# Performance work log

Measured on AMD Instinct MI355X. Metric: run time of the kernel, lower is better.

The kernel has to match this reference:

```python
import jax, jax.numpy as jnp
import numpy as np

N = 20000   # nodes
E = 640000  # edges
F = 128     # input feature dim
H1 = 64     # hidden1
H2 = 32     # hidden2 (forced by Bilinear(32,32,1))
R = 65      # num_relations / num classes
B = 4096    # query pairs


def rgcn_conv(x, src, dst, etype, W, Wroot, b):
    """PyG RGCNConv with aggr='mean': out_i = sum_r mean_{j in N_r(i)} x_j @ W_r + x_i @ Wroot + b."""
    n, f = x.shape
    seg = dst * R + etype                      # combined (node, relation) segment id
    msgs = x[src]                              # [E, f] gather
    agg = jax.ops.segment_sum(msgs, seg, num_segments=n * R).reshape(n, R, f)
    cnt = jax.ops.segment_sum(jnp.ones((msgs.shape[0],), x.dtype), seg, num_segments=n * R).reshape(n, R, 1)
    mean = agg / jnp.maximum(cnt, 1.0)         # mean per relation, zero where no edges
    out = jnp.einsum('nrf,rfo->no', mean, W) + x @ Wroot + b
    return out


def bilinear(h, c, w, b):
    # torch.nn.Bilinear(32,32,1): w [1,32,32], b [1]
    return jnp.einsum('nh,hk,nk->n', h, w[0], c)[:, None] + b


def setup_inputs():
    key = jax.random.key(0)
    ks = jax.random.split(key, 20)
    inp = {}
    inp['x_o'] = jax.random.normal(ks[0], (N, F), jnp.float32)
    inp['x_a'] = jax.random.normal(ks[1], (N, F), jnp.float32)
    inp['edge_index'] = jax.random.randint(ks[2], (2, E), 0, N, dtype=jnp.int32)
    inp['e_type'] = jax.random.randint(ks[3], (E,), 0, R, dtype=jnp.int32)
    inp['e_type1'] = jax.random.randint(ks[4], (E,), 0, R, dtype=jnp.int32)
    inp['idx'] = jax.random.randint(ks[5], (2, B), 0, N, dtype=jnp.int32)
    # RGCN layer 1
    s1 = 1.0 / np.sqrt(F)
    inp['W1'] = jax.random.normal(ks[6], (R, F, H1), jnp.float32) * s1
    inp['root1'] = jax.random.normal(ks[7], (F, H1), jnp.float32) * s1
    inp['b1'] = jnp.zeros((H1,), jnp.float32)
    # RGCN layer 2
    s2 = 1.0 / np.sqrt(H1)
    inp['W2'] = jax.random.normal(ks[8], (R, H1, H2), jnp.float32) * s2
    inp['root2'] = jax.random.normal(ks[9], (H1, H2), jnp.float32) * s2
    inp['b2'] = jnp.zeros((H2,), jnp.float32)
    # attention mix, discriminator, classifier
    inp['attt'] = jnp.array([0.5, 0.5], jnp.float32)
    inp['disc_w'] = jax.random.normal(ks[10], (1, H2, H2), jnp.float32) * (1.0 / np.sqrt(H2))
    inp['disc_b'] = jnp.zeros((1,), jnp.float32)
    cin = 2 * (H1 + H2)
    inp['cls_w'] = jax.random.normal(ks[11], (cin, R), jnp.float32) * (1.0 / np.sqrt(cin))
    inp['cls_b'] = jnp.zeros((R,), jnp.float32)
    return inp


def reference(x_o, x_a, edge_index, e_type, e_type1, idx,
              W1, root1, b1, W2, root2, b2, attt, disc_w, disc_b, cls_w, cls_b):
    src, dst = edge_index[0], edge_index[1]
    # three encoder passes (dropout is identity at eval)
    x1_o = jax.nn.relu(rgcn_conv(x_o, src, dst, e_type, W1, root1, b1))
    x2_o = rgcn_conv(x1_o, src, dst, e_type, W2, root2, b2)

    x1_a = jax.nn.relu(rgcn_conv(x_a, src, dst, e_type, W1, root1, b1))
    x2_o_a = rgcn_conv(x1_a, src, dst, e_type, W2, root2, b2)

    x1_aa = jax.nn.relu(rgcn_conv(x_o, src, dst, e_type1, W1, root1, b1))
    x2_o_a_a = rgcn_conv(x1_aa, src, dst, e_type1, W2, root2, b2)

    # readout + sigmoid, expanded summary vector
    h_os = jax.nn.sigmoid(jnp.mean(x2_o, axis=0))        # [H2]
    c_x = jnp.broadcast_to(h_os, x2_o.shape)             # [N, H2]
    ret_os = jnp.concatenate([bilinear(x2_o, c_x, disc_w, disc_b),
                              bilinear(x2_o_a, c_x, disc_w, disc_b)], axis=1)
    ret_os_a = jnp.concatenate([bilinear(x2_o, c_x, disc_w, disc_b),
                                bilinear(x2_o_a_a, c_x, disc_w, disc_b)], axis=1)

    final = jnp.concatenate([attt[0] * x1_o, attt[1] * x2_o], axis=1)  # [N, H1+H2]
    entity1 = final[idx[0]]
    entity2 = final[idx[1]]
    concat = jnp.concatenate([entity1, entity2], axis=1)  # [B, 2*(H1+H2)]
    log = concat @ cls_w + cls_b                           # [B, 65]
    return (log, ret_os, ret_os_a, x2_o)
```

## Files before the change

kernel.cpp:

```cpp
#include <hip/hip_runtime.h>

#define NN 20000
#define NE 640000
#define FF 128
#define H1 64
#define H2 32
#define RR 65
#define BQ 4096
#define NDPAD 20480

#define SM_HIST_A 0
#define SM_START_A 128
#define SM_CUR_A 256
#define SM_HIST_B 384
#define SM_START_B 512
#define SM_CUR_B 640
#define SM_HACC 768
#define SM_V 832

#define CPB1 32
#define CPB2 32

typedef __attribute__((ext_vector_type(8))) short bhalf8;
typedef __attribute__((ext_vector_type(4))) float f32x4;
// ... 1 lines not shown

__device__ __forceinline__ unsigned short f2bf(float f) {
  unsigned int u = __float_as_uint(f);
  unsigned int r = (u + 0x7fffu + ((u >> 16) & 1u)) >> 16;
  return (unsigned short)r;
}
__device__ __forceinline__ float bf2f(unsigned short u) {
  return __uint_as_float((unsigned)u << 16);
}
__device__ __forceinline__ void atomPK(unsigned short* p, unsigned v) {
  asm volatile("global_atomic_pk_add_bf16 %0, %1, off"
               :: "v"((unsigned long long)p), "v"(v) : "memory");
}

__global__ __launch_bounds__(256) void k_hist(
    const int* __restrict__ ei, const int* __restrict__ etA, const int* __restrict__ etB,
    int* __restrict__ sm, int* __restrict__ cntD) {
  __shared__ int lh[2 * RR];
  int tid = threadIdx.x;
  for (int i = tid; i < 2 * RR; i += blockDim.x) lh[i] = 0;
  __syncthreads();
  int e = blockIdx.x * blockDim.x + tid;
  if (e < NE) {
    int dst = ei[NE + e];
    atomicAdd(&cntD[dst], 1);
    atomicAdd(&lh[etA[e]], 1);
    atomicAdd(&lh[RR + etB[e]], 1);
  }
  __syncthreads();
  for (int i = tid; i < 2 * RR; i += blockDim.x) {
    int c = lh[i];
    if (c) atomicAdd(&sm[(i < RR) ? (SM_HIST_A + i) : (SM_HIST_B + (i - RR))], c);
  }
}

__global__ __launch_bounds__(128) void k_prefix(int* __restrict__ sm) {
  int w = threadIdx.x >> 6;
  if ((threadIdx.x & 63) == 0 && w < 2) {
    int hb = w ? SM_HIST_B : SM_HIST_A;
    int sb = w ? SM_START_B : SM_START_A;
    int cb = w ? SM_CUR_B : SM_CUR_A;
    int h[RR];
#pragma unroll
    for (int r = 0; r < RR; ++r) h[r] = sm[hb + r];
    int s = 0;
#pragma unroll
    for (int r = 0; r < RR; ++r) { sm[sb + r] = s; sm[cb + r] = s; s += h[r]; }
  }
}

__global__ __launch_bounds__(256) void k_prefixD(
    const int* __restrict__ cntD, int* __restrict__ startD,
    int* __restrict__ curA, int* __restrict__ curB) {
  __shared__ int psum[256];
  __shared__ int pbase[257];
  int t = threadIdx.x;
  int c0 = t * 80;
  int c1 = (c0 + 80 < NN) ? (c0 + 80) : NN;
  int s = 0;
  for (int i = c0; i < c1; ++i) s += cntD[i];
  psum[t] = s;
  __syncthreads();
  if (t == 0) {
    int a = 0;
    for (int i = 0; i < 256; ++i) { pbase[i] = a; a += psum[i]; }
    pbase[256] = a;
  }
  __syncthreads();
  int run = pbase[t];
  for (int i = c0; i < c1; ++i) {
    startD[i] = run; curA[i] = run; curB[i] = run;
    run += cntD[i];
  }
  if (t == 255) startD[NN] = pbase[256];
}

__global__ __launch_bounds__(256) void k_scatter(
    const int* __restrict__ etA, const int* __restrict__ etB,
    int* __restrict__ sm, int* __restrict__ ordA, int* __restrict__ ordB) {
  __shared__ int lhA[RR], lbA[RR], lhB[RR], lbB[RR];
  int tid = threadIdx.x;
  for (int i = tid; i < RR; i += blockDim.x) { lhA[i] = 0; lhB[i] = 0; }
  __syncthreads();
  int e = blockIdx.x * blockDim.x + tid;
  int ta = 0, tb = 0, ra = 0, rb = 0;
  bool valid = (e < NE);
  if (valid) {
    ta = etA[e]; tb = etB[e];
    ra = atomicAdd(&lhA[ta], 1);
    rb = atomicAdd(&lhB[tb], 1);
  }
  __syncthreads();
  for (int i = tid; i < RR; i += blockDim.x) {
    if (lhA[i]) lbA[i] = atomicAdd(&sm[SM_CUR_A + i], lhA[i]);
    if (lhB[i]) lbB[i] = atomicAdd(&sm[SM_CUR_B + i], lhB[i]);
  }
  __syncthreads();
  if (valid) { ordA[lbA[ta] + ra] = e; ordB[lbB[tb] + rb] = e; }
}

__global__ __launch_bounds__(256) void k_emeta(
    const int* __restrict__ ei, const int* __restrict__ ordA, const int* __restrict__ ordB,
    const int* __restrict__ etA, const int* __restrict__ etB,
    int2* __restrict__ sdA, int2* __restrict__ sdB) {
  int p = blockIdx.x * blockDim.x + threadIdx.x;
  if (p >= NE) return;
  {
    int e = ordA[p];
    sdA[p] = make_int2(ei[e] | (etA[e] << 20), ei[NE + e]);
  }
  {
    int e = ordB[p];
    sdB[p] = make_int2(ei[e] | (etB[e] << 20), ei[NE + e]);
  }
}

__global__ __launch_bounds__(256) void k_scatterD(
    const int2* __restrict__ sdA, const int2* __restrict__ sdB,
    int* __restrict__ curA, int* __restrict__ curB,
    int* __restrict__ posA, int* __restrict__ posB) {
  int p = blockIdx.x * blockDim.x + threadIdx.x;
  if (p >= NE) return;
  posA[atomicAdd(&curA[sdA[p].y], 1)] = p;
  posB[atomicAdd(&curB[sdB[p].y], 1)] = p;
}

__global__ __launch_bounds__(256) void k_invD(
    const int* __restrict__ startD, const int* __restrict__ pos,
    const int2* __restrict__ sd, float* __restrict__ iv) {
  int lane = threadIdx.x & 63;
  int d = (blockIdx.x * blockDim.x + threadIdx.x) >> 6;
  if (d >= NN) return;
  int e0 = startD[d], e1 = startD[d + 1];
  int len = e1 - e0;
  for (int c0 = 0; c0 < len; c0 += 64) {
    int myj = c0 + lane;
    int myp = 0, myrel = -1;
    if (myj < len) { myp = pos[e0 + myj]; myrel = ((unsigned)sd[myp].x) >> 20; }
    int cnt = 0;
    for (int c1 = 0; c1 < len; c1 += 64) {
      int oj = c1 + lane;
      int orel = (oj < len) ? (int)(((unsigned)sd[pos[e0 + oj]].x) >> 20) : -2;
      int kmax = (len - c1 < 64) ? (len - c1) : 64;
      for (int k = 0; k < kmax; ++k)
        cnt += (__shfl(orel, k) == myrel);
    }
    if (myj < len) iv[myp] = 1.0f / (float)cnt;
  }
}

__global__ __launch_bounds__(256) void k_cvt2(const float4* __restrict__ inA,
                                              const float4* __restrict__ inB,
                                              uint4* __restrict__ outA,
                                              uint4* __restrict__ outB, int n8) {
  int i = blockIdx.x * blockDim.x + threadIdx.x;
  if (i >= 2 * n8) return;
  const float4* in = (i < n8) ? inA : inB;
  uint4* out = (i < n8) ? outA : outB;
  int j = (i < n8) ? i : i - n8;
  float4 a = in[2 * j], b = in[2 * j + 1];
  uint4 o;
  o.x = (unsigned)f2bf(a.x) | ((unsigned)f2bf(a.y) << 16);
  o.y = (unsigned)f2bf(a.z) | ((unsigned)f2bf(a.w) << 16);
  o.z = (unsigned)f2bf(b.x) | ((unsigned)f2bf(b.y) << 16);
  o.w = (unsigned)f2bf(b.z) | ((unsigned)f2bf(b.w) << 16);
  out[j] = o;
}

__global__ __launch_bounds__(256) void k_relu16(uint4* __restrict__ a, int n4) {
  int i = blockIdx.x * blockDim.x + threadIdx.x;
// ... 53 lines not shown
#pragma unroll
  for (int j = 0; j < FF / 4; ++j) {
    float vo[4], va[4];
    *(float4*)vo = xo4[j];
    *(float4*)va = xa4[j];
#pragma unroll
    for (int t = 0; t < 4; ++t) {
      float wv = rt[(4 * j + t) * H1 + lane];
      so = fmaf(vo[t], wv, so);
      sa = fmaf(va[t], wv, sa);
    }
  }
  yo[(size_t)n * H1 + lane] = f2bf(so);
  yaa[(size_t)n * H1 + lane] = f2bf(so);
  ya[(size_t)n * H1 + lane] = f2bf(sa);
}

#define LM(G, SD, IV)                                       \
  {                                                         \
    const int base_ = s0 + ((G) << 4);                      \
    const int lim_ = cnt - ((G) << 4);                      \
    const int off_ = base_ + ((col < lim_) ? col : 0);      \
    SD = sdp[off_];                                         \
    IV = (col < lim_) ? invp[off_] : 0.f;                   \
  }

#define MFMA_BODY1(A0, A1, A2, A3)                                  \
  f32x4 c0 = {0.f,0.f,0.f,0.f}, c1 = c0, c2 = c0, c3 = c0;          \
  c0 = MFMA16(A0, wb[0], c0);  c1 = MFMA16(A0, wb[1], c1);          \
  c2 = MFMA16(A0, wb[2], c2);  c3 = MFMA16(A0, wb[3], c3);          \
  c0 = MFMA16(A1, wb[4], c0);  c1 = MFMA16(A1, wb[5], c1);          \
  c2 = MFMA16(A1, wb[6], c2);  c3 = MFMA16(A1, wb[7], c3);          \
  c0 = MFMA16(A2, wb[8], c0);  c1 = MFMA16(A2, wb[9], c1);          \
  c2 = MFMA16(A2, wb[10], c2); c3 = MFMA16(A2, wb[11], c3);         \
  c0 = MFMA16(A3, wb[12], c0); c1 = MFMA16(A3, wb[13], c1);         \
  c2 = MFMA16(A3, wb[14], c2); c3 = MFMA16(A3, wb[15], c3);

template <int NIN>
__global__ __launch_bounds__(256, 2) void k_edge1m(
    const int2* __restrict__ sdp, const float* __restrict__ invp,
    const int* __restrict__ sm, int startOff, int histOff,
    const unsigned short* __restrict__ Wf,
    const unsigned short* __restrict__ x16A, const unsigned short* __restrict__ x16B,
    unsigned short* __restrict__ yA, unsigned short* __restrict__ yB) {
  const int r = blockIdx.x / CPB1;
  const int lane = threadIdx.x & 63;
  bhalf8 wb[16];
  {
    const bhalf8* wf = (const bhalf8*)Wf + ((size_t)r * 16) * 64 + lane;
#pragma unroll
    for (int s = 0; s < 16; ++s) wb[s] = wf[(size_t)s * 64];
  }
  const int wvid = (blockIdx.x - r * CPB1) * 4 + (threadIdx.x >> 6);
  const int stride = CPB1 * 4;
  const int s0 = sm[startOff + r];
  const int cnt = sm[histOff + r];
  const int ngroups = (cnt + 15) >> 4;
  if (wvid >= ngroups) return;
  const int cg = lane >> 4;
  const int col = lane & 15;
  const int row0 = cg << 2;

  int2 sdC; float ivC;
  LM(wvid, sdC, ivC);
  for (int G = wvid; G < ngroups; G += stride) {
    int2 sdN = sdC; float ivN = ivC;
    if (G + stride < ngroups) LM(G + stride, sdN, ivN);
    const int src = sdC.x & 0xFFFFF;
    const int dstv = sdC.y;
    const int d0 = __shfl(dstv, row0),     d1 = __shfl(dstv, row0 + 1),
              d2 = __shfl(dstv, row0 + 2), d3 = __shfl(dstv, row0 + 3);
    const float i0 = __shfl(ivC, row0),     i1 = __shfl(ivC, row0 + 1),
                i2 = __shfl(ivC, row0 + 2), i3 = __shfl(ivC, row0 + 3);
#define SCAT1(Y, CCN, NOFF)                                                     \
    {                                                                           \
      float v0 = (CCN)[0] * i0, v1 = (CCN)[1] * i1,                             \
            v2 = (CCN)[2] * i2, v3 = (CCN)[3] * i3;                             \
      float p0 = __shfl_xor(v0, 1), p1 = __shfl_xor(v1, 1),                     \
            p2 = __shfl_xor(v2, 1), p3 = __shfl_xor(v3, 1);                     \
      if (!(lane & 1)) {                                                        \
        atomPK(Y + (size_t)d0 * H1 + (NOFF) + col, (unsigned)f2bf(v0) | ((unsigned)f2bf(p0) << 16)); \
        atomPK(Y + (size_t)d1 * H1 + (NOFF) + col, (unsigned)f2bf(v1) | ((unsigned)f2bf(p1) << 16)); \
        atomPK(Y + (size_t)d2 * H1 + (NOFF) + col, (unsigned)f2bf(v2) | ((unsigned)f2bf(p2) << 16)); \
        atomPK(Y + (size_t)d3 * H1 + (NOFF) + col, (unsigned)f2bf(v3) | ((unsigned)f2bf(p3) << 16)); \
      }                                                                         \
    }
    {
      const bhalf8* xr = (const bhalf8*)x16A + ((size_t)src << 4);
      bhalf8 a0 = xr[cg], a1 = xr[4 + cg], a2 = xr[8 + cg], a3 = xr[12 + cg];
      MFMA_BODY1(a0, a1, a2, a3)
      SCAT1(yA, c0, 0); SCAT1(yA, c1, 16); SCAT1(yA, c2, 32); SCAT1(yA, c3, 48);
    }
    if constexpr (NIN == 2) {
      const bhalf8* xr = (const bhalf8*)x16B + ((size_t)src << 4);
      bhalf8 a0 = xr[cg], a1 = xr[4 + cg], a2 = xr[8 + cg], a3 = xr[12 + cg];
      MFMA_BODY1(a0, a1, a2, a3)
      SCAT1(yB, c0, 0); SCAT1(yB, c1, 16); SCAT1(yB, c2, 32); SCAT1(yB, c3, 48);
    }
#undef SCAT1
    sdC = sdN; ivC = ivN;
  }
}

template <int NIN>
__global__ __launch_bounds__(256, 2) void k_edge1s(
    const int2* __restrict__ sdp, const float* __restrict__ invp,
    const int* __restrict__ sm, int startOff, int histOff,
    const unsigned short* __restrict__ Wf,
    const unsigned short* __restrict__ x16A, const unsigned short* __restrict__ x16B,
    unsigned short* __restrict__ tA, unsigned short* __restrict__ tB) {
  const int r = blockIdx.x / CPB1;
  const int lane = threadIdx.x & 63;
  bhalf8 wb[16];
  {
    const bhalf8* wf = (const bhalf8*)Wf + ((size_t)r * 16) * 64 + lane;
#pragma unroll
    for (int s = 0; s < 16; ++s) wb[s] = wf[(size_t)s * 64];
  }
  const int wvid = (blockIdx.x - r * CPB1) * 4 + (threadIdx.x >> 6);
  const int stride = CPB1 * 4;
  const int s0 = sm[startOff + r];
  const int cnt = sm[histOff + r];
  const int ngroups = (cnt + 15) >> 4;
  if (wvid >= ngroups) return;
  const int cg = lane >> 4;
  const int col = lane & 15;
  const int row0 = cg << 2;

  int2 sdC; float ivC;
  LM(wvid, sdC, ivC);
  for (int G = wvid; G < ngroups; G += stride) {
    int2 sdN = sdC; float ivN = ivC;
    if (G + stride < ngroups) LM(G + stride, sdN, ivN);
    const int src = sdC.x & 0xFFFFF;
    const int base = s0 + (G << 4);
    const int lim = cnt - (G << 4);
    const float i0 = __shfl(ivC, row0),     i1 = __shfl(ivC, row0 + 1),
                i2 = __shfl(ivC, row0 + 2), i3 = __shfl(ivC, row0 + 3);
#define STOR1(T, CCN, NOFF)                                                     \
    {                                                                           \
      float v0 = (CCN)[0] * i0, v1 = (CCN)[1] * i1,                             \
            v2 = (CCN)[2] * i2, v3 = (CCN)[3] * i3;                             \
      float p0 = __shfl_xor(v0, 1), p1 = __shfl_xor(v1, 1),                     \
            p2 = __shfl_xor(v2, 1), p3 = __shfl_xor(v3, 1);                     \
      if (!(lane & 1)) {                                                        \
        if (row0 + 0 < lim) *(unsigned*)(T + (size_t)(base + row0 + 0) * H1 + (NOFF) + col) = (unsigned)f2bf(v0) | ((unsigned)f2bf(p0) << 16); \
        if (row0 + 1 < lim) *(unsigned*)(T + (size_t)(base + row0 + 1) * H1 + (NOFF) + col) = (unsigned)f2bf(v1) | ((unsigned)f2bf(p1) << 16); \
        if (row0 + 2 < lim) *(unsigned*)(T + (size_t)(base + row0 + 2) * H1 + (NOFF) + col) = (unsigned)f2bf(v2) | ((unsigned)f2bf(p2) << 16); \
        if (row0 + 3 < lim) *(unsigned*)(T + (size_t)(base + row0 + 3) * H1 + (NOFF) + col) = (unsigned)f2bf(v3) | ((unsigned)f2bf(p3) << 16); \
      }                                                                         \
    }
    {
      const bhalf8* xr = (const bhalf8*)x16A + ((size_t)src << 4);
      bhalf8 a0 = xr[cg], a1 = xr[4 + cg], a2 = xr[8 + cg], a3 = xr[12 + cg];
      MFMA_BODY1(a0, a1, a2, a3)
      STOR1(tA, c0, 0); STOR1(tA, c1, 16); STOR1(tA, c2, 32); STOR1(tA, c3, 48);
    }
    if constexpr (NIN == 2) {
      const bhalf8* xr = (const bhalf8*)x16B + ((size_t)src << 4);
      bhalf8 a0 = xr[cg], a1 = xr[4 + cg], a2 = xr[8 + cg], a3 = xr[12 + cg];
      MFMA_BODY1(a0, a1, a2, a3)
      STOR1(tB, c0, 0); STOR1(tB, c1, 16); STOR1(tB, c2, 32); STOR1(tB, c3, 48);
    }
#undef STOR1
    sdC = sdN; ivC = ivN;
  }
}

template <int NT>
__global__ __launch_bounds__(256) void k_reduce1(
    const int* __restrict__ startD, const int* __restrict__ pos,
    const unsigned short* __restrict__ t0, const unsigned short* __restrict__ t1,
    const unsigned short* __restrict__ r0, const unsigned short* __restrict__ r1,
    unsigned short* __restrict__ y0, unsigned short* __restrict__ y1) {
  int lane = threadIdx.x & 63;
  int d = (blockIdx.x * blockDim.x + threadIdx.x) >> 6;
  if (d >= NN) return;
  int e0 = startD[d], e1 = startD[d + 1];
  float a0 = 0.f, a1 = 0.f;
  int j = e0;
  for (; j + 4 <= e1; j += 4) {
    int p0 = pos[j], p1 = pos[j + 1], p2 = pos[j + 2], p3 = pos[j + 3];
    a0 += bf2f(t0[(size_t)p0 * H1 + lane]) + bf2f(t0[(size_t)p1 * H1 + lane])
        + bf2f(t0[(size_t)p2 * H1 + lane]) + bf2f(t0[(size_t)p3 * H1 + lane]);
    if constexpr (NT == 2)
      a1 += bf2f(t1[(size_t)p0 * H1 + lane]) + bf2f(t1[(size_t)p1 * H1 + lane])
          + bf2f(t1[(size_t)p2 * H1 + lane]) + bf2f(t1[(size_t)p3 * H1 + lane]);
  }
  for (; j < e1; ++j) {
    int p = pos[j];
    a0 += bf2f(t0[(size_t)p * H1 + lane]);
    if constexpr (NT == 2) a1 += bf2f(t1[(size_t)p * H1 + lane]);
  }
  size_t o = (size_t)d * H1 + lane;
  y0[o] = f2bf(fmaxf(bf2f(r0[o]) + a0, 0.f));
  if constexpr (NT == 2) y1[o] = f2bf(fmaxf(bf2f(r1[o]) + a1, 0.f));
}

__global__ __launch_bounds__(256) void k_root2x3(
    const unsigned short* __restrict__ x1o, const unsigned short* __restrict__ x1a,
    const unsigned short* __restrict__ x1aa,
    const float* __restrict__ rt, const float* __restrict__ b,
    unsigned short* __restrict__ y0, unsigned short* __restrict__ y1,
    unsigned short* __restrict__ y2) {
  int i = blockIdx.x * blockDim.x + threadIdx.x;
  if (i >= NN * H2) return;
  int o = i & (H2 - 1);
  int n = i >> 5;
  const uint2* p0 = (const uint2*)(x1o + (size_t)n * H1);
  const uint2* p1 = (const uint2*)(x1a + (size_t)n * H1);
  const uint2* p2 = (const uint2*)(x1aa + (size_t)n * H1);
  float s0 = b[o], s1 = s0, s2 = s0;
#pragma unroll
  for (int j = 0; j < 16; ++j) {
    uint2 u0 = p0[j], u1 = p1[j], u2 = p2[j];
#pragma unroll
    for (int t = 0; t < 4; ++t) {
      unsigned w0 = (t < 2) ? u0.x : u0.y;
      unsigned w1 = (t < 2) ? u1.x : u1.y;
      unsigned w2 = (t < 2) ? u2.x : u2.y;
      int sh = (t & 1) * 16;
      float wv = rt[(4 * j + t) * H2 + o];
      s0 = fmaf(bf2f((unsigned short)(w0 >> sh)), wv, s0);
      s1 = fmaf(bf2f((unsigned short)(w1 >> sh)), wv, s1);
      s2 = fmaf(bf2f((unsigned short)(w2 >> sh)), wv, s2);
    }
  }
  y0[i] = f2bf(s0); y1[i] = f2bf(s1); y2[i] = f2bf(s2);
}

template <int NIN>
__global__ __launch_bounds__(256, 2) void k_edge2m(
    const int2* __restrict__ sdp, const float* __restrict__ invp,
    const int* __restrict__ sm, int startOff, int histOff,
    const unsigned short* __restrict__ Wf,
    const unsigned short* __restrict__ x16A, const unsigned short* __restrict__ x16B,
    unsigned short* __restrict__ yA, unsigned short* __restrict__ yB) {
  const int r = blockIdx.x / CPB2;
  const int lane = threadIdx.x & 63;
  bhalf8 wb[4];
  {
    const bhalf8* wf = (const bhalf8*)Wf + ((size_t)r * 4) * 64 + lane;
#pragma unroll
    for (int s = 0; s < 4; ++s) wb[s] = wf[(size_t)s * 64];
  }
  const int wvid = (blockIdx.x - r * CPB2) * 4 + (threadIdx.x >> 6);
  const int stride = CPB2 * 4;
  const int s0 = sm[startOff + r];
  const int cnt = sm[histOff + r];
  const int ngroups = (cnt + 15) >> 4;
  if (wvid >= ngroups) return;
  const int cg = lane >> 4;
  const int col = lane & 15;
  const int row0 = cg << 2;

  int2 sdC; float ivC;
  LM(wvid, sdC, ivC);
  for (int G = wvid; G < ngroups; G += stride) {
    int2 sdN = sdC; float ivN = ivC;
    if (G + stride < ngroups) LM(G + stride, sdN, ivN);
    const int src = sdC.x & 0xFFFFF;
    const int dstv = sdC.y;
    const int d0 = __shfl(dstv, row0),     d1 = __shfl(dstv, row0 + 1),
              d2 = __shfl(dstv, row0 + 2), d3 = __shfl(dstv, row0 + 3);
    const float i0 = __shfl(ivC, row0),     i1 = __shfl(ivC, row0 + 1),
                i2 = __shfl(ivC, row0 + 2), i3 = __shfl(ivC, row0 + 3);
#define SCAT2(Y, CCN, NOFF)                                                     \
    {                                                                           \
      float v0 = (CCN)[0] * i0, v1 = (CCN)[1] * i1,                             \
            v2 = (CCN)[2] * i2, v3 = (CCN)[3] * i3;                             \
      float p0 = __shfl_xor(v0, 1), p1 = __shfl_xor(v1, 1),                     \
            p2 = __shfl_xor(v2, 1), p3 = __shfl_xor(v3, 1);                     \
      if (!(lane & 1)) {                                                        \
        atomPK(Y + (size_t)d0 * H2 + (NOFF) + col, (unsigned)f2bf(v0) | ((unsigned)f2bf(p0) << 16)); \
        atomPK(Y + (size_t)d1 * H2 + (NOFF) + col, (unsigned)f2bf(v1) | ((unsigned)f2bf(p1) << 16)); \
        atomPK(Y + (size_t)d2 * H2 + (NOFF) + col, (unsigned)f2bf(v2) | ((unsigned)f2bf(p2) << 16)); \
        atomPK(Y + (size_t)d3 * H2 + (NOFF) + col, (unsigned)f2bf(v3) | ((unsigned)f2bf(p3) << 16)); \
      }                                                                         \
    }
    {
      const bhalf8* xr = (const bhalf8*)x16A + ((size_t)src << 3);
      bhalf8 a0 = xr[cg], a1 = xr[4 + cg];
      f32x4 c0 = {0.f,0.f,0.f,0.f}, c1 = c0;
      c0 = MFMA16(a0, wb[0], c0); c1 = MFMA16(a0, wb[1], c1);
      c0 = MFMA16(a1, wb[2], c0); c1 = MFMA16(a1, wb[3], c1);
      SCAT2(yA, c0, 0); SCAT2(yA, c1, 16);
    }
    if constexpr (NIN == 2) {
      const bhalf8* xr = (const bhalf8*)x16B + ((size_t)src << 3);
      bhalf8 a0 = xr[cg], a1 = xr[4 + cg];
      f32x4 c0 = {0.f,0.f,0.f,0.f}, c1 = c0;
      c0 = MFMA16(a0, wb[0], c0); c1 = MFMA16(a0, wb[1], c1);
      c0 = MFMA16(a1, wb[2], c0); c1 = MFMA16(a1, wb[3], c1);
      SCAT2(yB, c0, 0); SCAT2(yB, c1, 16);
    }
#undef SCAT2
    sdC = sdN; ivC = ivN;
  }
}

template <int NIN>
__global__ __launch_bounds__(256, 2) void k_edge2s(
    const int2* __restrict__ sdp, const float* __restrict__ invp,
    const int* __restrict__ sm, int startOff, int histOff,
    const unsigned short* __restrict__ Wf,
    const unsigned short* __restrict__ x16A, const unsigned short* __restrict__ x16B,
    unsigned short* __restrict__ tA, unsigned short* __restrict__ tB) {
  const int r = blockIdx.x / CPB2;
  const int lane = threadIdx.x & 63;
  bhalf8 wb[4];
  {
    const bhalf8* wf = (const bhalf8*)Wf + ((size_t)r * 4) * 64 + lane;
#pragma unroll
    for (int s = 0; s < 4; ++s) wb[s] = wf[(size_t)s * 64];
  }
  const int wvid = (blockIdx.x - r * CPB2) * 4 + (threadIdx.x >> 6);
  const int stride = CPB2 * 4;
  const int s0 = sm[startOff + r];
  const int cnt = sm[histOff + r];
  const int ngroups = (cnt + 15) >> 4;
  if (wvid >= ngroups) return;
  const int cg = lane >> 4;
  const int col = lane & 15;
  const int row0 = cg << 2;

  int2 sdC; float ivC;
  LM(wvid, sdC, ivC);
  for (int G = wvid; G < ngroups; G += stride) {
    int2 sdN = sdC; float ivN = ivC;
    if (G + stride < ngroups) LM(G + stride, sdN, ivN);
    const int src = sdC.x & 0xFFFFF;
    const int base = s0 + (G << 4);
    const int lim = cnt - (G << 4);
    const float i0 = __shfl(ivC, row0),     i1 = __shfl(ivC, row0 + 1),
                i2 = __shfl(ivC, row0 + 2), i3 = __shfl(ivC, row0 + 3);
#define STOR2(T, CCN, NOFF)                                                     \
    {                                                                           \
      float v0 = (CCN)[0] * i0, v1 = (CCN)[1] * i1,                             \
            v2 = (CCN)[2] * i2, v3 = (CCN)[3] * i3;                             \
      float p0 = __shfl_xor(v0, 1), p1 = __shfl_xor(v1, 1),                     \
            p2 = __shfl_xor(v2, 1), p3 = __shfl_xor(v3, 1);                     \
      if (!(lane & 1)) {                                                        \
        if (row0 + 0 < lim) *(unsigned*)(T + (size_t)(base + row0 + 0) * H2 + (NOFF) + col) = (unsigned)f2bf(v0) | ((unsigned)f2bf(p0) << 16); \
        if (row0 + 1 < lim) *(unsigned*)(T + (size_t)(base + row0 + 1) * H2 + (NOFF) + col) = (unsigned)f2bf(v1) | ((unsigned)f2bf(p1) << 16); \
        if (row0 + 2 < lim) *(unsigned*)(T + (size_t)(base + row0 + 2) * H2 + (NOFF) + col) = (unsigned)f2bf(v2) | ((unsigned)f2bf(p2) << 16); \
        if (row0 + 3 < lim) *(unsigned*)(T + (size_t)(base + row0 + 3) * H2 + (NOFF) + col) = (unsigned)f2bf(v3) | ((unsigned)f2bf(p3) << 16); \
      }                                                                         \
    }
    {
      const bhalf8* xr = (const bhalf8*)x16A + ((size_t)src << 3);
      bhalf8 a0 = xr[cg], a1 = xr[4 + cg];
      f32x4 c0 = {0.f,0.f,0.f,0.f}, c1 = c0;
      c0 = MFMA16(a0, wb[0], c0); c1 = MFMA16(a0, wb[1], c1);
      c0 = MFMA16(a1, wb[2], c0); c1 = MFMA16(a1, wb[3], c1);
      STOR2(tA, c0, 0); STOR2(tA, c1, 16);
    }
    if constexpr (NIN == 2) {
      const bhalf8* xr = (const bhalf8*)x16B + ((size_t)src << 3);
      bhalf8 a0 = xr[cg], a1 = xr[4 + cg];
      f32x4 c0 = {0.f,0.f,0.f,0.f}, c1 = c0;
      c0 = MFMA16(a0, wb[0], c0); c1 = MFMA16(a0, wb[1], c1);
      c0 = MFMA16(a1, wb[2], c0); c1 = MFMA16(a1, wb[3], c1);
      STOR2(tB, c0, 0); STOR2(tB, c1, 16);
    }
#undef STOR2
    sdC = sdN; ivC = ivN;
  }
}

template <int NT>
__global__ __launch_bounds__(256) void k_reduce2(
    const int* __restrict__ startD, const int* __restrict__ pos,
    const unsigned short* __restrict__ t0, const unsigned short* __restrict__ t1,
    const unsigned short* __restrict__ r0, const unsigned short* __restrict__ r1,
    unsigned short* __restrict__ y0, unsigned short* __restrict__ y1,
    float* __restrict__ f32out) {
  int gt = blockIdx.x * blockDim.x + threadIdx.x;
  int d = gt >> 5;
  int colc = gt & 31;
  if (d >= NN) return;
  int e0 = startD[d], e1 = startD[d + 1];
  float a0 = 0.f, a1 = 0.f;
  int j = e0;
  for (; j + 4 <= e1; j += 4) {
    int p0 = pos[j], p1 = pos[j + 1], p2 = pos[j + 2], p3 = pos[j + 3];
    a0 += bf2f(t0[(size_t)p0 * H2 + colc]) + bf2f(t0[(size_t)p1 * H2 + colc])
        + bf2f(t0[(size_t)p2 * H2 + colc]) + bf2f(t0[(size_t)p3 * H2 + colc]);
    if constexpr (NT == 2)
      a1 += bf2f(t1[(size_t)p0 * H2 + colc]) + bf2f(t1[(size_t)p1 * H2 + colc])
          + bf2f(t1[(size_t)p2 * H2 + colc]) + bf2f(t1[(size_t)p3 * H2 + colc]);
  }
  for (; j < e1; ++j) {
    int p = pos[j];
    a0 += bf2f(t0[(size_t)p * H2 + colc]);
    if constexpr (NT == 2) a1 += bf2f(t1[(size_t)p * H2 + colc]);
  }
  size_t o = (size_t)d * H2 + colc;
  float v0 = bf2f(r0[o]) + a0;
  y0[o] = f2bf(v0);
  if (f32out) f32out[o] = v0;
  if constexpr (NT == 2) y1[o] = f2bf(bf2f(r1[o]) + a1);
}

__global__ __launch_bounds__(256) void k_fin(const uint4* __restrict__ xb,
                                             float4* __restrict__ out, int n8) {
  int i = blockIdx.x * blockDim.x + threadIdx.x;
  if (i >= n8) return;
  uint4 u = xb[i];
  float4 a, b;
  a.x = bf2f((unsigned short)u.x); a.y = bf2f((unsigned short)(u.x >> 16));
  a.z = bf2f((unsigned short)u.y); a.w = bf2f((unsigned short)(u.y >> 16));
  b.x = bf2f((unsigned short)u.z); b.y = bf2f((unsigned short)(u.z >> 16));
  b.z = bf2f((unsigned short)u.w); b.w = bf2f((unsigned short)(u.w >> 16));
  out[2 * i] = a; out[2 * i + 1] = b;
}

__global__ __launch_bounds__(256) void k_colsum(const float* __restrict__ x2o,
                                                float* __restrict__ hacc) {
// ... 104 lines not shown
                              hipStream_t stream) {
  const float* x_o  = (const float*)d_in[0];
  const float* x_a  = (const float*)d_in[1];
  const int*   ei   = (const int*)d_in[2];
  const int*   etA  = (const int*)d_in[3];
  const int*   etB  = (const int*)d_in[4];
  const int*   idx  = (const int*)d_in[5];
  const float* W1   = (const float*)d_in[6];
  const float* rt1  = (const float*)d_in[7];
  const float* b1   = (const float*)d_in[8];
  const float* W2   = (const float*)d_in[9];
  const float* rt2  = (const float*)d_in[10];
  const float* b2   = (const float*)d_in[11];
  const float* attt = (const float*)d_in[12];
  const float* dw   = (const float*)d_in[13];
  const float* db   = (const float*)d_in[14];
  const float* cw   = (const float*)d_in[15];
  const float* cb   = (const float*)d_in[16];

  int* wsI    = (int*)d_ws;
  int* sm     = wsI;
  int* cntD   = sm + 1024;
  int* startD = cntD + NDPAD;
  int* curA   = startD + NDPAD;
  int* curB   = curA + NDPAD;
  int* ordA   = curB + NDPAD;
  int* ordB   = ordA + NE;
  int* posA   = ordB + NE;
  int* posB   = posA + NE;
  int2*  sdA  = (int2*)(posB + NE);
  int2*  sdB  = sdA + NE;
  float* ivA  = (float*)(sdB + NE);
  float* ivB  = ivA + NE;
  unsigned short* x1o16   = (unsigned short*)(ivB + NE);
  unsigned short* x1a16   = x1o16 + (size_t)NN * H1;
  unsigned short* x1aa16  = x1a16 + (size_t)NN * H1;
  unsigned short* x2ob    = x1aa16 + (size_t)NN * H1;
  unsigned short* x2oab   = x2ob + (size_t)NN * H2;
  unsigned short* x2oaab  = x2oab + (size_t)NN * H2;
  unsigned short* xo16    = x2oaab + (size_t)NN * H2;
  unsigned short* xa16    = xo16 + (size_t)NN * FF;
  unsigned short* W1f     = xa16 + (size_t)NN * FF;
  unsigned short* W2f     = W1f + (size_t)RR * 16 * 64 * 8;
  unsigned short* rootO16 = W2f + (size_t)RR * 4 * 64 * 8;
  unsigned short* rootA16 = rootO16 + (size_t)NN * H1;
  unsigned short* r2o16   = rootA16 + (size_t)NN * H1;
  unsigned short* r2a16   = r2o16 + (size_t)NN * H2;
  unsigned short* r2aa16  = r2a16 + (size_t)NN * H2;
  unsigned short* t0      = r2aa16 + (size_t)NN * H2;
  unsigned short* t1      = t0 + (size_t)NE * H1;
  unsigned short* tc1     = t0 + (size_t)NE * H2;

  const size_t ofsT = (size_t)((char*)t0 - (char*)d_ws);
  const size_t needFull = ofsT + (size_t)2 * NE * H1 * 2 + 256;
  const size_t needMid  = ofsT + (size_t)2 * NE * H2 * 2 + 256;
  const bool fullT = ws_size >= needFull;
  const bool midT  = fullT || ws_size >= needMid;

  float* smF  = (float*)sm;
  float* hacc = smF + SM_HACC;
  float* vbuf = smF + SM_V;

  float* outF   = (float*)d_out;
  float* o_log  = outF;
  float* o_ros  = outF + (size_t)BQ * RR;
  float* o_rosa = o_ros + (size_t)NN * 2;
  float* o_x2o  = o_rosa + (size_t)NN * 2;

  hipMemsetAsync(wsI, 0, (1024 + NDPAD) * sizeof(int), stream);

  k_cvt2<<<(2 * NN * FF / 8 + 255) / 256, 256, 0, stream>>>(
      (const float4*)x_o, (const float4*)x_a, (uint4*)xo16, (uint4*)xa16, NN * FF / 8);
  k_wprep1<<<RR, 256, 0, stream>>>(W1, W1f);
  k_wprep2<<<RR, 256, 0, stream>>>(W2, W2f);

  k_hist<<<(NE + 255) / 256, 256, 0, stream>>>(ei, etA, etB, sm, cntD);
  k_prefix<<<1, 128, 0, stream>>>(sm);
  k_prefixD<<<1, 256, 0, stream>>>(cntD, startD, curA, curB);
  k_scatter<<<(NE + 255) / 256, 256, 0, stream>>>(etA, etB, sm, ordA, ordB);
  k_emeta<<<(NE + 255) / 256, 256, 0, stream>>>(ei, ordA, ordB, etA, etB, sdA, sdB);
  k_scatterD<<<(NE + 255) / 256, 256, 0, stream>>>(sdA, sdB, curA, curB, posA, posB);
  k_invD<<<(NN * 64 + 255) / 256, 256, 0, stream>>>(startD, posA, sdA, ivA);
  k_invD<<<(NN * 64 + 255) / 256, 256, 0, stream>>>(startD, posB, sdB, ivB);

  if (fullT) {
    k_root1<<<(NN * H1) / 256, 256, 0, stream>>>(x_o, x_a, rt1, b1,
                                                 rootO16, rootO16, rootA16);
    k_edge1s<2><<<RR * CPB1, 256, 0, stream>>>(sdA, ivA, sm, SM_START_A, SM_HIST_A,
                                               W1f, xo16, xa16, t0, t1);
    k_reduce1<2><<<(NN * 64) / 256, 256, 0, stream>>>(startD, posA, t0, t1,
                                                      rootO16, rootA16, x1o16, x1a16);
    k_edge1s<1><<<RR * CPB1, 256, 0, stream>>>(sdB, ivB, sm, SM_START_B, SM_HIST_B,
                                               W1f, xo16, nullptr, t0, nullptr);
    k_reduce1<1><<<(NN * 64) / 256, 256, 0, stream>>>(startD, posB, t0, nullptr,
                                                      rootO16, nullptr, x1aa16, nullptr);
  } else {
    k_root1<<<(NN * H1) / 256, 256, 0, stream>>>(x_o, x_a, rt1, b1,
                                                 x1o16, x1aa16, x1a16);
    k_edge1m<2><<<RR * CPB1, 256, 0, stream>>>(sdA, ivA, sm, SM_START_A, SM_HIST_A,
                                               W1f, xo16, xa16, x1o16, x1a16);
    k_edge1m<1><<<RR * CPB1, 256, 0, stream>>>(sdB, ivB, sm, SM_START_B, SM_HIST_B,
                                               W1f, xo16, nullptr, x1aa16, nullptr);
    k_relu16<<<(3 * NN * H1 / 8 + 255) / 256, 256, 0, stream>>>((uint4*)x1o16,
                                                                3 * NN * H1 / 8);
  }

  if (midT) {
    k_root2x3<<<(NN * H2 + 255) / 256, 256, 0, stream>>>(x1o16, x1a16, x1aa16, rt2, b2,
                                                         r2o16, r2a16, r2aa16);
    k_edge2s<2><<<RR * CPB2, 256, 0, stream>>>(sdA, ivA, sm, SM_START_A, SM_HIST_A,
                                               W2f, x1o16, x1a16, t0, tc1);
    k_reduce2<2><<<(NN * 32) / 256, 256, 0, stream>>>(startD, posA, t0, tc1,
                                                      r2o16, r2a16, x2ob, x2oab, o_x2o);
    k_edge2s<1><<<RR * CPB2, 256, 0, stream>>>(sdB, ivB, sm, SM_START_B, SM_HIST_B,
                                               W2f, x1aa16, nullptr, t0, nullptr);
    k_reduce2<1><<<(NN * 32) / 256, 256, 0, stream>>>(startD, posB, t0, nullptr,
                                                      r2aa16, nullptr, x2oaab, nullptr,
                                                      nullptr);
  } else {
    k_root2x3<<<(NN * H2 + 255) / 256, 256, 0, stream>>>(x1o16, x1a16, x1aa16, rt2, b2,
                                                         x2ob, x2oab, x2oaab);
    k_edge2m<2><<<RR * CPB2, 256, 0, stream>>>(sdA, ivA, sm, SM_START_A, SM_HIST_A,
                                               W2f, x1o16, x1a16, x2ob, x2oab);
    k_edge2m<1><<<RR * CPB2, 256, 0, stream>>>(sdB, ivB, sm, SM_START_B, SM_HIST_B,
                                               W2f, x1aa16, nullptr, x2oaab, nullptr);
    k_fin<<<(NN * H2 / 8 + 255) / 256, 256, 0, stream>>>((const uint4*)x2ob,
                                                         (float4*)o_x2o, NN * H2 / 8);
  }

  k_colsum<<<128, 256, 0, stream>>>(o_x2o, hacc);
  k_disc<<<1, 64, 0, stream>>>(hacc, dw, vbuf);
  k_ret<<<(NN + 255) / 256, 256, 0, stream>>>(x2ob, x2oab, x2oaab, vbuf, db, o_ros, o_rosa);
  k_cls<<<BQ, 128, 0, stream>>>(idx, x1o16, o_x2o, attt, cw, cb, o_log);
}
```

Measured before the change: 828.1 us.

## Fuse edge preprocessing into one scatter with shared destination-slot index

Replaces the scatter, edge-metadata, destination-scatter and two inverse-count kernels with a single fused scatter. That scatter assigns each edge one destination-sorted slot q and packs src and dst into 15 bits each. Edge kernels write messages directly to slot q, so the reduce kernels read contiguous rows instead of chasing a pos indirection. A combined relation array lets one pass compute the inverse counts for both edge-type sets. This removes several launches and indirect loads, in exchange for scattered stores in the edge kernels and a 15-bit packing limit on node ids.

```diff
diff --git a/kernel.cpp b/kernel.cpp
--- a/kernel.cpp
+++ b/kernel.cpp
@@ -47,8 +47,7 @@
   __syncthreads();
   int e = blockIdx.x * blockDim.x + tid;
   if (e < NE) {
-    int dst = ei[NE + e];
-    atomicAdd(&cntD[dst], 1);
+    atomicAdd(&cntD[ei[NE + e]], 1);
     atomicAdd(&lh[etA[e]], 1);
     atomicAdd(&lh[RR + etB[e]], 1);
   }
@@ -75,8 +74,7 @@
 }
 
 __global__ __launch_bounds__(256) void k_prefixD(
-    const int* __restrict__ cntD, int* __restrict__ startD,
-    int* __restrict__ curA, int* __restrict__ curB) {
+    const int* __restrict__ cntD, int* __restrict__ startD, int* __restrict__ cur) {
   __shared__ int psum[256];
   __shared__ int pbase[257];
   int t = threadIdx.x;
@@ -94,15 +92,17 @@
   __syncthreads();
   int run = pbase[t];
   for (int i = c0; i < c1; ++i) {
-    startD[i] = run; curA[i] = run; curB[i] = run;
+    startD[i] = run; cur[i] = run;
     run += cntD[i];
   }
   if (t == 255) startD[NN] = pbase[256];
 }
 
-__global__ __launch_bounds__(256) void k_scatter(
-    const int* __restrict__ etA, const int* __restrict__ etB,
-    int* __restrict__ sm, int* __restrict__ ordA, int* __restrict__ ordB) {
+__global__ __launch_bounds__(256) void k_scatterF(
+    const int* __restrict__ ei, const int* __restrict__ etA, const int* __restrict__ etB,
+    int* __restrict__ sm, int* __restrict__ cur,
+    int2* __restrict__ sdA, int2* __restrict__ sdB,
+    unsigned short* __restrict__ relQ) {
   __shared__ int lhA[RR], lbA[RR], lhB[RR], lbB[RR];
   int tid = threadIdx.x;
   for (int i = tid; i < RR; i += blockDim.x) { lhA[i] = 0; lhB[i] = 0; }
@@ -121,38 +121,19 @@
     if (lhB[i]) lbB[i] = atomicAdd(&sm[SM_CUR_B + i], lhB[i]);
   }
   __syncthreads();
-  if (valid) { ordA[lbA[ta] + ra] = e; ordB[lbB[tb] + rb] = e; }
-}
-
-__global__ __launch_bounds__(256) void k_emeta(
-    const int* __restrict__ ei, const int* __restrict__ ordA, const int* __restrict__ ordB,
-    const int* __restrict__ etA, const int* __restrict__ etB,
-    int2* __restrict__ sdA, int2* __restrict__ sdB) {
-  int p = blockIdx.x * blockDim.x + threadIdx.x;
-  if (p >= NE) return;
-  {
-    int e = ordA[p];
-    sdA[p] = make_int2(ei[e] | (etA[e] << 20), ei[NE + e]);
-  }
-  {
-    int e = ordB[p];
-    sdB[p] = make_int2(ei[e] | (etB[e] << 20), ei[NE + e]);
-  }
-}
-
-__global__ __launch_bounds__(256) void k_scatterD(
-    const int2* __restrict__ sdA, const int2* __restrict__ sdB,
-    int* __restrict__ curA, int* __restrict__ curB,
-    int* __restrict__ posA, int* __restrict__ posB) {
-  int p = blockIdx.x * blockDim.x + threadIdx.x;
-  if (p >= NE) return;
-  posA[atomicAdd(&curA[sdA[p].y], 1)] = p;
-  posB[atomicAdd(&curB[sdB[p].y], 1)] = p;
-}
-
-__global__ __launch_bounds__(256) void k_invD(
-    const int* __restrict__ startD, const int* __restrict__ pos,
-    const int2* __restrict__ sd, float* __restrict__ iv) {
+  if (valid) {
+    int src = ei[e], dst = ei[NE + e];
+    int q = atomicAdd(&cur[dst], 1);
+    int packed = src | (dst << 15);
+    sdA[lbA[ta] + ra] = make_int2(packed, q);
+    sdB[lbB[tb] + rb] = make_int2(packed, q);
+    relQ[q] = (unsigned short)(ta | (tb << 8));
+  }
+}
+
+__global__ __launch_bounds__(256) void k_invD2(
+    const int* __restrict__ startD, const unsigned short* __restrict__ relQ,
+    float* __restrict__ ivqA, float* __restrict__ ivqB) {
   int lane = threadIdx.x & 63;
   int d = (blockIdx.x * blockDim.x + threadIdx.x) >> 6;
   if (d >= NN) return;
@@ -160,17 +141,23 @@
   int len = e1 - e0;
   for (int c0 = 0; c0 < len; c0 += 64) {
     int myj = c0 + lane;
-    int myp = 0, myrel = -1;
-    if (myj < len) { myp = pos[e0 + myj]; myrel = ((unsigned)sd[myp].x) >> 20; }
-    int cnt = 0;
+    int mr = (myj < len) ? (int)relQ[e0 + myj] : 0;
+    int mA = mr & 0xFF, mB = mr >> 8;
+    int cA = 0, cB = 0;
     for (int c1 = 0; c1 < len; c1 += 64) {
       int oj = c1 + lane;
-      int orel = (oj < len) ? (int)(((unsigned)sd[pos[e0 + oj]].x) >> 20) : -2;
+      int orr = (oj < len) ? (int)relQ[e0 + oj] : 0;
       int kmax = (len - c1 < 64) ? (len - c1) : 64;
-      for (int k = 0; k < kmax; ++k)
-        cnt += (__shfl(orel, k) == myrel);
-    }
-    if (myj < len) iv[myp] = 1.0f / (float)cnt;
+      for (int k = 0; k < kmax; ++k) {
+        int o = __shfl(orr, k);
+        cA += ((o & 0xFF) == mA);
+        cB += ((o >> 8) == mB);
+      }
+    }
+    if (myj < len) {
+      ivqA[e0 + myj] = 1.0f / (float)cA;
+      ivqB[e0 + myj] = 1.0f / (float)cB;
+    }
   }
 }
 
@@ -270,7 +257,7 @@
     const int lim_ = cnt - ((G) << 4);                      \
     const int off_ = base_ + ((col < lim_) ? col : 0);      \
     SD = sdp[off_];                                         \
-    IV = (col < lim_) ? invp[off_] : 0.f;                   \
+    IV = (col < lim_) ? ivq[SD.y] : 0.f;                    \
   }
 
 #define MFMA_BODY1(A0, A1, A2, A3)                                  \
@@ -286,7 +273,7 @@
 
 template <int NIN>
 __global__ __launch_bounds__(256, 2) void k_edge1m(
-    const int2* __restrict__ sdp, const float* __restrict__ invp,
+    const int2* __restrict__ sdp, const float* __restrict__ ivq,
     const int* __restrict__ sm, int startOff, int histOff,
     const unsigned short* __restrict__ Wf,
     const unsigned short* __restrict__ x16A, const unsigned short* __restrict__ x16B,
@@ -314,8 +301,8 @@
   for (int G = wvid; G < ngroups; G += stride) {
     int2 sdN = sdC; float ivN = ivC;
     if (G + stride < ngroups) LM(G + stride, sdN, ivN);
-    const int src = sdC.x & 0xFFFFF;
-    const int dstv = sdC.y;
+    const int src = sdC.x & 0x7FFF;
+    const int dstv = (sdC.x >> 15) & 0x7FFF;
     const int d0 = __shfl(dstv, row0),     d1 = __shfl(dstv, row0 + 1),
               d2 = __shfl(dstv, row0 + 2), d3 = __shfl(dstv, row0 + 3);
     const float i0 = __shfl(ivC, row0),     i1 = __shfl(ivC, row0 + 1),
@@ -352,7 +339,7 @@
 
 template <int NIN>
 __global__ __launch_bounds__(256, 2) void k_edge1s(
-    const int2* __restrict__ sdp, const float* __restrict__ invp,
+    const int2* __restrict__ sdp, const float* __restrict__ ivq,
     const int* __restrict__ sm, int startOff, int histOff,
     const unsigned short* __restrict__ Wf,
     const unsigned short* __restrict__ x16A, const unsigned short* __restrict__ x16B,
@@ -380,9 +367,11 @@
   for (int G = wvid; G < ngroups; G += stride) {
     int2 sdN = sdC; float ivN = ivC;
     if (G + stride < ngroups) LM(G + stride, sdN, ivN);
-    const int src = sdC.x & 0xFFFFF;
-    const int base = s0 + (G << 4);
+    const int src = sdC.x & 0x7FFF;
+    const int qv = sdC.y;
     const int lim = cnt - (G << 4);
+    const int q0 = __shfl(qv, row0),     q1 = __shfl(qv, row0 + 1),
+              q2 = __shfl(qv, row0 + 2), q3 = __shfl(qv, row0 + 3);
     const float i0 = __shfl(ivC, row0),     i1 = __shfl(ivC, row0 + 1),
                 i2 = __shfl(ivC, row0 + 2), i3 = __shfl(ivC, row0 + 3);
 #define STOR1(T, CCN, NOFF)                                                     \
@@ -392,10 +381,10 @@
       float p0 = __shfl_xor(v0, 1), p1 = __shfl_xor(v1, 1),                     \
             p2 = __shfl_xor(v2, 1), p3 = __shfl_xor(v3, 1);                     \
       if (!(lane & 1)) {                                                        \
-        if (row0 + 0 < lim) *(unsigned*)(T + (size_t)(base + row0 + 0) * H1 + (NOFF) + col) = (unsigned)f2bf(v0) | ((unsigned)f2bf(p0) << 16); \
-        if (row0 + 1 < lim) *(unsigned*)(T + (size_t)(base + row0 + 1) * H1 + (NOFF) + col) = (unsigned)f2bf(v1) | ((unsigned)f2bf(p1) << 16); \
-        if (row0 + 2 < lim) *(unsigned*)(T + (size_t)(base + row0 + 2) * H1 + (NOFF) + col) = (unsigned)f2bf(v2) | ((unsigned)f2bf(p2) << 16); \
-        if (row0 + 3 < lim) *(unsigned*)(T + (size_t)(base + row0 + 3) * H1 + (NOFF) + col) = (unsigned)f2bf(v3) | ((unsigned)f2bf(p3) << 16); \
+        if (row0 + 0 < lim) *(unsigned*)(T + (size_t)q0 * H1 + (NOFF) + col) = (unsigned)f2bf(v0) | ((unsigned)f2bf(p0) << 16); \
+        if (row0 + 1 < lim) *(unsigned*)(T + (size_t)q1 * H1 + (NOFF) + col) = (unsigned)f2bf(v1) | ((unsigned)f2bf(p1) << 16); \
+        if (row0 + 2 < lim) *(unsigned*)(T + (size_t)q2 * H1 + (NOFF) + col) = (unsigned)f2bf(v2) | ((unsigned)f2bf(p2) << 16); \
+        if (row0 + 3 < lim) *(unsigned*)(T + (size_t)q3 * H1 + (NOFF) + col) = (unsigned)f2bf(v3) | ((unsigned)f2bf(p3) << 16); \
       }                                                                         \
     }
     {
@@ -417,7 +406,7 @@
 
 template <int NT>
 __global__ __launch_bounds__(256) void k_reduce1(
-    const int* __restrict__ startD, const int* __restrict__ pos,
+    const int* __restrict__ startD,
     const unsigned short* __restrict__ t0, const unsigned short* __restrict__ t1,
     const unsigned short* __restrict__ r0, const unsigned short* __restrict__ r1,
     unsigned short* __restrict__ y0, unsigned short* __restrict__ y1) {
@@ -426,19 +415,9 @@
   if (d >= NN) return;
   int e0 = startD[d], e1 = startD[d + 1];
   float a0 = 0.f, a1 = 0.f;
-  int j = e0;
-  for (; j + 4 <= e1; j += 4) {
-    int p0 = pos[j], p1 = pos[j + 1], p2 = pos[j + 2], p3 = pos[j + 3];
-    a0 += bf2f(t0[(size_t)p0 * H1 + lane]) + bf2f(t0[(size_t)p1 * H1 + lane])
-        + bf2f(t0[(size_t)p2 * H1 + lane]) + bf2f(t0[(size_t)p3 * H1 + lane]);
-    if constexpr (NT == 2)
-      a1 += bf2f(t1[(size_t)p0 * H1 + lane]) + bf2f(t1[(size_t)p1 * H1 + lane])
-          + bf2f(t1[(size_t)p2 * H1 + lane]) + bf2f(t1[(size_t)p3 * H1 + lane]);
-  }
-  for (; j < e1; ++j) {
-    int p = pos[j];
-    a0 += bf2f(t0[(size_t)p * H1 + lane]);
-    if constexpr (NT == 2) a1 += bf2f(t1[(size_t)p * H1 + lane]);
+  for (int j = e0; j < e1; ++j) {
+    a0 += bf2f(t0[(size_t)j * H1 + lane]);
+    if constexpr (NT == 2) a1 += bf2f(t1[(size_t)j * H1 + lane]);
   }
   size_t o = (size_t)d * H1 + lane;
   y0[o] = f2bf(fmaxf(bf2f(r0[o]) + a0, 0.f));
@@ -479,7 +458,7 @@
 
 template <int NIN>
 __global__ __launch_bounds__(256, 2) void k_edge2m(
-    const int2* __restrict__ sdp, const float* __restrict__ invp,
+    const int2* __restrict__ sdp, const float* __restrict__ ivq,
     const int* __restrict__ sm, int startOff, int histOff,
     const unsigned short* __restrict__ Wf,
     const unsigned short* __restrict__ x16A, const unsigned short* __restrict__ x16B,
@@ -507,8 +486,8 @@
   for (int G = wvid; G < ngroups; G += stride) {
     int2 sdN = sdC; float ivN = ivC;
     if (G + stride < ngroups) LM(G + stride, sdN, ivN);
-    const int src = sdC.x & 0xFFFFF;
-    const int dstv = sdC.y;
+    const int src = sdC.x & 0x7FFF;
+    const int dstv = (sdC.x >> 15) & 0x7FFF;
     const int d0 = __shfl(dstv, row0),     d1 = __shfl(dstv, row0 + 1),
               d2 = __shfl(dstv, row0 + 2), d3 = __shfl(dstv, row0 + 3);
     const float i0 = __shfl(ivC, row0),     i1 = __shfl(ivC, row0 + 1),
@@ -549,7 +528,7 @@
 
 template <int NIN>
 __global__ __launch_bounds__(256, 2) void k_edge2s(
-    const int2* __restrict__ sdp, const float* __restrict__ invp,
+    const int2* __restrict__ sdp, const float* __restrict__ ivq,
     const int* __restrict__ sm, int startOff, int histOff,
     const unsigned short* __restrict__ Wf,
     const unsigned short* __restrict__ x16A, const unsigned short* __restrict__ x16B,
@@ -577,9 +556,11 @@
   for (int G = wvid; G < ngroups; G += stride) {
     int2 sdN = sdC; float ivN = ivC;
     if (G + stride < ngroups) LM(G + stride, sdN, ivN);
-    const int src = sdC.x & 0xFFFFF;
-    const int base = s0 + (G << 4);
+    const int src = sdC.x & 0x7FFF;
+    const int qv = sdC.y;
     const int lim = cnt - (G << 4);
+    const int q0 = __shfl(qv, row0),     q1 = __shfl(qv, row0 + 1),
+              q2 = __shfl(qv, row0 + 2), q3 = __shfl(qv, row0 + 3);
     const float i0 = __shfl(ivC, row0),     i1 = __shfl(ivC, row0 + 1),
                 i2 = __shfl(ivC, row0 + 2), i3 = __shfl(ivC, row0 + 3);
 #define STOR2(T, CCN, NOFF)                                                     \
@@ -589,10 +570,10 @@
       float p0 = __shfl_xor(v0, 1), p1 = __shfl_xor(v1, 1),                     \
             p2 = __shfl_xor(v2, 1), p3 = __shfl_xor(v3, 1);                     \
       if (!(lane & 1)) {                                                        \
-        if (row0 + 0 < lim) *(unsigned*)(T + (size_t)(base + row0 + 0) * H2 + (NOFF) + col) = (unsigned)f2bf(v0) | ((unsigned)f2bf(p0) << 16); \
-        if (row0 + 1 < lim) *(unsigned*)(T + (size_t)(base + row0 + 1) * H2 + (NOFF) + col) = (unsigned)f2bf(v1) | ((unsigned)f2bf(p1) << 16); \
-        if (row0 + 2 < lim) *(unsigned*)(T + (size_t)(base + row0 + 2) * H2 + (NOFF) + col) = (unsigned)f2bf(v2) | ((unsigned)f2bf(p2) << 16); \
-        if (row0 + 3 < lim) *(unsigned*)(T + (size_t)(base + row0 + 3) * H2 + (NOFF) + col) = (unsigned)f2bf(v3) | ((unsigned)f2bf(p3) << 16); \
+        if (row0 + 0 < lim) *(unsigned*)(T + (size_t)q0 * H2 + (NOFF) + col) = (unsigned)f2bf(v0) | ((unsigned)f2bf(p0) << 16); \
+        if (row0 + 1 < lim) *(unsigned*)(T + (size_t)q1 * H2 + (NOFF) + col) = (unsigned)f2bf(v1) | ((unsigned)f2bf(p1) << 16); \
+        if (row0 + 2 < lim) *(unsigned*)(T + (size_t)q2 * H2 + (NOFF) + col) = (unsigned)f2bf(v2) | ((unsigned)f2bf(p2) << 16); \
+        if (row0 + 3 < lim) *(unsigned*)(T + (size_t)q3 * H2 + (NOFF) + col) = (unsigned)f2bf(v3) | ((unsigned)f2bf(p3) << 16); \
       }                                                                         \
     }
     {
@@ -618,7 +599,7 @@
 
 template <int NT>
 __global__ __launch_bounds__(256) void k_reduce2(
-    const int* __restrict__ startD, const int* __restrict__ pos,
+    const int* __restrict__ startD,
     const unsigned short* __restrict__ t0, const unsigned short* __restrict__ t1,
     const unsigned short* __restrict__ r0, const unsigned short* __restrict__ r1,
     unsigned short* __restrict__ y0, unsigned short* __restrict__ y1,
@@ -629,19 +610,9 @@
   if (d >= NN) return;
   int e0 = startD[d], e1 = startD[d + 1];
   float a0 = 0.f, a1 = 0.f;
-  int j = e0;
-  for (; j + 4 <= e1; j += 4) {
-    int p0 = pos[j], p1 = pos[j + 1], p2 = pos[j + 2], p3 = pos[j + 3];
-    a0 += bf2f(t0[(size_t)p0 * H2 + colc]) + bf2f(t0[(size_t)p1 * H2 + colc])
-        + bf2f(t0[(size_t)p2 * H2 + colc]) + bf2f(t0[(size_t)p3 * H2 + colc]);
-    if constexpr (NT == 2)
-      a1 += bf2f(t1[(size_t)p0 * H2 + colc]) + bf2f(t1[(size_t)p1 * H2 + colc])
-          + bf2f(t1[(size_t)p2 * H2 + colc]) + bf2f(t1[(size_t)p3 * H2 + colc]);
-  }
-  for (; j < e1; ++j) {
-    int p = pos[j];
-    a0 += bf2f(t0[(size_t)p * H2 + colc]);
-    if constexpr (NT == 2) a1 += bf2f(t1[(size_t)p * H2 + colc]);
+  for (int j = e0; j < e1; ++j) {
+    a0 += bf2f(t0[(size_t)j * H2 + colc]);
+    if constexpr (NT == 2) a1 += bf2f(t1[(size_t)j * H2 + colc]);
   }
   size_t o = (size_t)d * H2 + colc;
   float v0 = bf2f(r0[o]) + a0;
@@ -792,17 +763,13 @@
   int* sm     = wsI;
   int* cntD   = sm + 1024;
   int* startD = cntD + NDPAD;
-  int* curA   = startD + NDPAD;
-  int* curB   = curA + NDPAD;
-  int* ordA   = curB + NDPAD;
-  int* ordB   = ordA + NE;
-  int* posA   = ordB + NE;
-  int* posB   = posA + NE;
-  int2*  sdA  = (int2*)(posB + NE);
+  int* cur    = startD + NDPAD;
+  unsigned short* relQ = (unsigned short*)(cur + NDPAD);
+  int2*  sdA  = (int2*)((int*)(relQ + NE) + (NE & 1));
   int2*  sdB  = sdA + NE;
-  float* ivA  = (float*)(sdB + NE);
-  float* ivB  = ivA + NE;
-  unsigned short* x1o16   = (unsigned short*)(ivB + NE);
+  float* ivqA = (float*)(sdB + NE);
+  float* ivqB = ivqA + NE;
+  unsigned short* x1o16   = (unsigned short*)(ivqB + NE);
   unsigned short* x1a16   = x1o16 + (size_t)NN * H1;
   unsigned short* x1aa16  = x1a16 + (size_t)NN * H1;
   unsigned short* x2ob    = x1aa16 + (size_t)NN * H1;
@@ -846,30 +813,28 @@
 
   k_hist<<<(NE + 255) / 256, 256, 0, stream>>>(ei, etA, etB, sm, cntD);
   k_prefix<<<1, 128, 0, stream>>>(sm);
-  k_prefixD<<<1, 256, 0, stream>>>(cntD, startD, curA, curB);
-  k_scatter<<<(NE + 255) / 256, 256, 0, stream>>>(etA, etB, sm, ordA, ordB);
-  k_emeta<<<(NE + 255) / 256, 256, 0, stream>>>(ei, ordA, ordB, etA, etB, sdA, sdB);
-  k_scatterD<<<(NE + 255) / 256, 256, 0, stream>>>(sdA, sdB, curA, curB, posA, posB);
-  k_invD<<<(NN * 64 + 255) / 256, 256, 0, stream>>>(startD, posA, sdA, ivA);
-  k_invD<<<(NN * 64 + 255) / 256, 256, 0, stream>>>(startD, posB, sdB, ivB);
+  k_prefixD<<<1, 256, 0, stream>>>(cntD, startD, cur);
+  k_scatterF<<<(NE + 255) / 256, 256, 0, stream>>>(ei, etA, etB, sm, cur,
+                                                   sdA, sdB, relQ);
+  k_invD2<<<(NN * 64 + 255) / 256, 256, 0, stream>>>(startD, relQ, ivqA, ivqB);
 
   if (fullT) {
     k_root1<<<(NN * H1) / 256, 256, 0, stream>>>(x_o, x_a, rt1, b1,
                                                  rootO16, rootO16, rootA16);
-    k_edge1s<2><<<RR * CPB1, 256, 0, stream>>>(sdA, ivA, sm, SM_START_A, SM_HIST_A,
+    k_edge1s<2><<<RR * CPB1, 256, 0, stream>>>(sdA, ivqA, sm, SM_START_A, SM_HIST_A,
                                                W1f, xo16, xa16, t0, t1);
-    k_reduce1<2><<<(NN * 64) / 256, 256, 0, stream>>>(startD, posA, t0, t1,
+    k_reduce1<2><<<(NN * 64) / 256, 256, 0, stream>>>(startD, t0, t1,
                                                       rootO16, rootA16, x1o16, x1a16);
-    k_edge1s<1><<<RR * CPB1, 256, 0, stream>>>(sdB, ivB, sm, SM_START_B, SM_HIST_B,
+    k_edge1s<1><<<RR * CPB1, 256, 0, stream>>>(sdB, ivqB, sm, SM_START_B, SM_HIST_B,
                                                W1f, xo16, nullptr, t0, nullptr);
-    k_reduce1<1><<<(NN * 64) / 256, 256, 0, stream>>>(startD, posB, t0, nullptr,
+    k_reduce1<1><<<(NN * 64) / 256, 256, 0, stream>>>(startD, t0, nullptr,
                                                       rootO16, nullptr, x1aa16, nullptr);
   } else {
     k_root1<<<(NN * H1) / 256, 256, 0, stream>>>(x_o, x_a, rt1, b1,
                                                  x1o16, x1aa16, x1a16);
-    k_edge1m<2><<<RR * CPB1, 256, 0, stream>>>(sdA, ivA, sm, SM_START_A, SM_HIST_A,
+    k_edge1m<2><<<RR * CPB1, 256, 0, stream>>>(sdA, ivqA, sm, SM_START_A, SM_HIST_A,
                                                W1f, xo16, xa16, x1o16, x1a16);
-    k_edge1m<1><<<RR * CPB1, 256, 0, stream>>>(sdB, ivB, sm, SM_START_B, SM_HIST_B,
+    k_edge1m<1><<<RR * CPB1, 256, 0, stream>>>(sdB, ivqB, sm, SM_START_B, SM_HIST_B,
                                                W1f, xo16, nullptr, x1aa16, nullptr);
     k_relu16<<<(3 * NN * H1 / 8 + 255) / 256, 256, 0, stream>>>((uint4*)x1o16,
                                                                 3 * NN * H1 / 8);
@@ -878,21 +843,21 @@
   if (midT) {
     k_root2x3<<<(NN * H2 + 255) / 256, 256, 0, stream>>>(x1o16, x1a16, x1aa16, rt2, b2,
                                                          r2o16, r2a16, r2aa16);
-    k_edge2s<2><<<RR * CPB2, 256, 0, stream>>>(sdA, ivA, sm, SM_START_A, SM_HIST_A,
+    k_edge2s<2><<<RR * CPB2, 256, 0, stream>>>(sdA, ivqA, sm, SM_START_A, SM_HIST_A,
                                                W2f, x1o16, x1a16, t0, tc1);
-    k_reduce2<2><<<(NN * 32) / 256, 256, 0, stream>>>(startD, posA, t0, tc1,
+    k_reduce2<2><<<(NN * 32) / 256, 256, 0, stream>>>(startD, t0, tc1,
                                                       r2o16, r2a16, x2ob, x2oab, o_x2o);
-    k_edge2s<1><<<RR * CPB2, 256, 0, stream>>>(sdB, ivB, sm, SM_START_B, SM_HIST_B,
+    k_edge2s<1><<<RR * CPB2, 256, 0, stream>>>(sdB, ivqB, sm, SM_START_B, SM_HIST_B,
                                                W2f, x1aa16, nullptr, t0, nullptr);
-    k_reduce2<1><<<(NN * 32) / 256, 256, 0, stream>>>(startD, posB, t0, nullptr,
+    k_reduce2<1><<<(NN * 32) / 256, 256, 0, stream>>>(startD, t0, nullptr,
                                                       r2aa16, nullptr, x2oaab, nullptr,
                                                       nullptr);
   } else {
     k_root2x3<<<(NN * H2 + 255) / 256, 256, 0, stream>>>(x1o16, x1a16, x1aa16, rt2, b2,
                                                          x2ob, x2oab, x2oaab);
-    k_edge2m<2><<<RR * CPB2, 256, 0, stream>>>(sdA, ivA, sm, SM_START_A, SM_HIST_A,
+    k_edge2m<2><<<RR * CPB2, 256, 0, stream>>>(sdA, ivqA, sm, SM_START_A, SM_HIST_A,
                                                W2f, x1o16, x1a16, x2ob, x2oab);
-    k_edge2m<1><<<RR * CPB2, 256, 0, stream>>>(sdB, ivB, sm, SM_START_B, SM_HIST_B,
+    k_edge2m<1><<<RR * CPB2, 256, 0, stream>>>(sdB, ivqB, sm, SM_START_B, SM_HIST_B,
                                                W2f, x1aa16, nullptr, x2oaab, nullptr);
     k_fin<<<(NN * H2 / 8 + 255) / 256, 256, 0, stream>>>((const uint4*)x2ob,
                                                          (float4*)o_x2o, NN * H2 / 8);
```

New measurement: 740.0 us, median of 2. 10.6% less time.
